# Kernel tuning notes

Hardware: AMD Instinct MI355X
Metric: run time of the kernel (lower is better)

## Reference

```python
import jax, jax.numpy as jnp
import numpy as np

BLOCK_SIZE = 64          # elements per quantization block
SCALER_BLOCK_SIZE = 256  # scalers per double-quantization block
OUT, IN = 11008, 4096
N_BLOCKS = OUT * IN // BLOCK_SIZE          # 704512
N_SCALER_BLOCKS = N_BLOCKS // SCALER_BLOCK_SIZE  # 2752

# QLoRA NF4 (4-bit NormalFloat) codebook
NF4_TABLE = np.array([
    -1.0, -0.6961928009986877, -0.5250730514526367, -0.39491748809814453,
    -0.28444138169288635, -0.18477343022823334, -0.10644006729125977,
    -0.029167551919817924, 0.0, 0.07958029955625534, 0.16093020141124725,
    0.24611230194568634, 0.33791524171829224, 0.44070982933044434,
    0.5626170039176941, 0.7229568362236023], dtype=np.float32)


def setup_inputs() -> dict:
    key = jax.random.key(0)
    k1, k2, k3, k4, k5 = jax.random.split(key, 5)
    x = jax.random.normal(k1, (4, 2048, IN), dtype=jnp.float32)
    # 4-bit codebook indices for each weight element
    qweight = jax.random.randint(k2, (OUT, IN), 0, 16, dtype=jnp.int32)
    # int8-style quantized per-block scalers (positive magnitudes)
    quantized_scalers = jax.random.randint(k3, (N_BLOCKS,), 1, 127, dtype=jnp.int32)
    # per scaler-block quantization factor (strictly positive, away from zero)
    quantization_factor = jax.random.uniform(k4, (N_SCALER_BLOCKS,), dtype=jnp.float32,
                                             minval=0.5, maxval=1.5) * 127.0
    scaler_mean = jax.random.uniform(k5, (1,), dtype=jnp.float32) * 0.01
    return {"x": x, "qweight": qweight, "quantized_scalers": quantized_scalers,
            "quantization_factor": quantization_factor, "scaler_mean": scaler_mean}


def dequantize_nf4(qweight, quantized_scalers, quantization_factor, scaler_mean, dtype):
    table = jnp.asarray(NF4_TABLE, dtype=dtype)
    # double-dequantize the per-block scalers
    scalers = (quantized_scalers.astype(dtype)
               / jnp.repeat(quantization_factor.astype(dtype), SCALER_BLOCK_SIZE)
               + scaler_mean.astype(dtype)[0])                      # [N_BLOCKS]
    # codebook lookup, then per-block scale
    w = table[qweight].reshape(N_BLOCKS, BLOCK_SIZE) * scalers[:, None]
    return w.reshape(OUT, IN)


def reference(x, qweight, quantized_scalers, quantization_factor, scaler_mean):
    # Faithful to LinearNF4.forward: F.linear(x, weight.to(x.dtype))
    w = dequantize_nf4(qweight, quantized_scalers, quantization_factor,
                       scaler_mean, x.dtype)                        # [OUT, IN]
    return jnp.einsum('bsi,oi->bso', x, w)
```

## Files before the change

### kernel.cpp

```cpp
#include <hip/hip_runtime.h>
#include <stdint.h>

#define M_ROWS 8192
#define K_DIM  4096
#define N_DIM  11008
#define KSTEPS (K_DIM / 64)

#define BM 256
#define BN 256
#define MBLKS (M_ROWS / BM)
#define NBLKS (N_DIM / BN)
#define NWG   (MBLKS * NBLKS)

typedef __attribute__((ext_vector_type(4))) float          f32x4;
typedef __attribute__((ext_vector_type(8))) __bf16         bf16x8;
typedef __attribute__((ext_vector_type(4))) int            i32x4;
typedef __attribute__((ext_vector_type(8))) unsigned short u16x8;

__constant__ float NF4_TBL[16] = {
    -1.0f, -0.6961928009986877f, -0.5250730514526367f, -0.39491748809814453f,
    -0.28444138169288635f, -0.18477343022823334f, -0.10644006729125977f,
    -0.029167551919817924f, 0.0f, 0.07958029955625534f, 0.16093020141124725f,
    0.24611230194568634f, 0.33791524171829224f, 0.44070982933044434f,
    0.5626170039176941f, 0.7229568362236023f};

__device__ __forceinline__ unsigned short f2bf(float f) {
  uint32_t u = __float_as_uint(f);
  u += 0x7fffu + ((u >> 16) & 1u);
  return (unsigned short)(u >> 16);
}

__device__ __forceinline__ void gload_lds16(const void* g, const void* l) {
  __builtin_amdgcn_global_load_lds(
      (const __attribute__((address_space(1))) void*)(uintptr_t)g,
      (__attribute__((address_space(3))) void*)(uint32_t)(uintptr_t)l,
      16, 0, 0);
}

__global__ void convert_x_kernel(const float* __restrict__ x,
                                 unsigned short* __restrict__ xb) {
  const long n8 = (long)M_ROWS * K_DIM / 8;
  for (long t = (long)blockIdx.x * blockDim.x + threadIdx.x; t < n8;
       t += (long)gridDim.x * blockDim.x) {
    const float* p = x + t * 8;
    f32x4 v0 = *(const f32x4*)p;
    f32x4 v1 = *(const f32x4*)(p + 4);
    u16x8 o;
    o[0] = f2bf(v0[0]); o[1] = f2bf(v0[1]); o[2] = f2bf(v0[2]); o[3] = f2bf(v0[3]);
    o[4] = f2bf(v1[0]); o[5] = f2bf(v1[1]); o[6] = f2bf(v1[2]); o[7] = f2bf(v1[3]);
    *(u16x8*)(xb + t * 8) = o;
  }
}

__global__ void dequant_w_kernel(const int* __restrict__ qw,
                                 const int* __restrict__ qs,
                                 const float* __restrict__ qf,
                                 const float* __restrict__ mean,
                                 unsigned short* __restrict__ wb) {
  __shared__ float tbl[16];
  if (threadIdx.x < 16) tbl[threadIdx.x] = NF4_TBL[threadIdx.x];
  __syncthreads();
  const float mu = mean[0];
  const long n8 = (long)N_DIM * K_DIM / 8;
  for (long t = (long)blockIdx.x * blockDim.x + threadIdx.x; t < n8;
       t += (long)gridDim.x * blockDim.x) {
    long f = t * 8;
    int  g = (int)(f >> 6);
    float s = (float)qs[g] / qf[g >> 8] + mu;
    i32x4 q0 = *(const i32x4*)(qw + f);
    i32x4 q1 = *(const i32x4*)(qw + f + 4);
    u16x8 o;
    o[0] = f2bf(tbl[q0[0]] * s); o[1] = f2bf(tbl[q0[1]] * s);
    o[2] = f2bf(tbl[q0[2]] * s); o[3] = f2bf(tbl[q0[3]] * s);
    o[4] = f2bf(tbl[q1[0]] * s); o[5] = f2bf(tbl[q1[1]] * s);
    o[6] = f2bf(tbl[q1[2]] * s); o[7] = f2bf(tbl[q1[3]] * s);
    *(u16x8*)(wb + f) = o;
  }
}

#define STG(GP, LB)                                                              \
  gload_lds16((GP) + (long)srow * K_DIM + scol, &LDSbuf[(LB) + wid * 1024]);     \
  gload_lds16((GP) + (long)(64 + srow) * K_DIM + scol,                           \
              &LDSbuf[(LB) + 8192 + wid * 1024]);

#define SB __builtin_amdgcn_sched_barrier(0)

#define RD_A2(DST, MB, SA)                                                        \
  DST[0][0] = *(const bf16x8*)&LDSbuf[(SA) + aoff + (MB) * 2048 + kswz0];         \
  DST[0][1] = *(const bf16x8*)&LDSbuf[(SA) + aoff + (MB) * 2048 + kswz1];         \
  DST[1][0] = *(const bf16x8*)&LDSbuf[(SA) + aoff + ((MB) + 1) * 2048 + kswz0];   \
  DST[1][1] = *(const bf16x8*)&LDSbuf[(SA) + aoff + ((MB) + 1) * 2048 + kswz1];

#define RD_B2(NB, CB)                                                             \
  bq[NB][0]     = *(const bf16x8*)&LDSbuf[(CB) + boff + (NB) * 2048 + kswz0];     \
  bq[NB][1]     = *(const bf16x8*)&LDSbuf[(CB) + boff + (NB) * 2048 + kswz1];     \
  bq[NB + 1][0] = *(const bf16x8*)&LDSbuf[(CB) + boff + ((NB) + 1) * 2048 + kswz0];\
  bq[NB + 1][1] = *(const bf16x8*)&LDSbuf[(CB) + boff + ((NB) + 1) * 2048 + kswz1];

#define MFP(MI, AF, AI, NI)                                                       \
  acc[MI][NI] = __builtin_amdgcn_mfma_f32_16x16x32_bf16(AF[AI][0], bq[NI][0], acc[MI][NI], 0, 0, 0); \
  acc[MI][NI] = __builtin_amdgcn_mfma_f32_16x16x32_bf16(AF[AI][1], bq[NI][1], acc[MI][NI], 0, 0, 0);

#define TILE_BODY(BASE)                                                           \
    RD_A2(af_a, ((BASE) + 0) & 7, sAr);                                           \
    RD_B2(0, cB);                                                                 \
    SB;                                                                           \
    RD_B2(2, cB);                                                                 \
    STG(wb + n0g * K_DIM + kB, nB);                                               \
    __builtin_amdgcn_s_setprio(1);                                                \
    MFP(((BASE) + 0) & 7, af_a, 0, 0) MFP(((BASE) + 1) & 7, af_a, 1, 0)           \
    MFP(((BASE) + 0) & 7, af_a, 0, 1) MFP(((BASE) + 1) & 7, af_a, 1, 1)           \
    __builtin_amdgcn_s_setprio(0);                                                \
    SB;                                                                           \
    RD_A2(af_b, ((BASE) + 2) & 7, sAr);                                           \
    STG(wb + (n0g + 128) * K_DIM + kB, nB + 16384);                               \
    __builtin_amdgcn_s_setprio(1);                                                \
    MFP(((BASE) + 0) & 7, af_a, 0, 2) MFP(((BASE) + 1) & 7, af_a, 1, 2)           \
    MFP(((BASE) + 0) & 7, af_a, 0, 3) MFP(((BASE) + 1) & 7, af_a, 1, 3)           \
    __builtin_amdgcn_s_setprio(0);                                                \
    SB;                                                                           \
    STG(xb + m0g * K_DIM + kA, sAs);                                              \
    __builtin_amdgcn_s_setprio(1);                                                \
    MFP(((BASE) + 2) & 7, af_b, 0, 2) MFP(((BASE) + 3) & 7, af_b, 1, 2)           \
    MFP(((BASE) + 2) & 7, af_b, 0, 3) MFP(((BASE) + 3) & 7, af_b, 1, 3)           \
    __builtin_amdgcn_s_setprio(0);                                                \
    SB;                                                                           \
    RD_A2(af_a, ((BASE) + 4) & 7, sAr);                                           \
    STG(xb + (m0g + 128) * K_DIM + kA, sAs + 16384);                              \
    __builtin_amdgcn_s_setprio(1);                                                \
    MFP(((BASE) + 2) & 7, af_b, 0, 0) MFP(((BASE) + 3) & 7, af_b, 1, 0)           \
    MFP(((BASE) + 2) & 7, af_b, 0, 1) MFP(((BASE) + 3) & 7, af_b, 1, 1)           \
    __builtin_amdgcn_s_setprio(0);                                                \
    SB;                                                                           \
    __builtin_amdgcn_s_setprio(1);                                                \
    MFP(((BASE) + 4) & 7, af_a, 0, 0) MFP(((BASE) + 5) & 7, af_a, 1, 0)           \
    MFP(((BASE) + 4) & 7, af_a, 0, 1) MFP(((BASE) + 5) & 7, af_a, 1, 1)           \
    __builtin_amdgcn_s_setprio(0);                                                \
    SB;                                                                           \
    RD_A2(af_b, ((BASE) + 6) & 7, sAr);                                           \
    __builtin_amdgcn_s_setprio(1);                                                \
    MFP(((BASE) + 4) & 7, af_a, 0, 2) MFP(((BASE) + 5) & 7, af_a, 1, 2)           \
    MFP(((BASE) + 4) & 7, af_a, 0, 3) MFP(((BASE) + 5) & 7, af_a, 1, 3)           \
    __builtin_amdgcn_s_setprio(0);                                                \
    SB;                                                                           \
    __builtin_amdgcn_s_setprio(1);                                                \
    MFP(((BASE) + 6) & 7, af_b, 0, 2) MFP(((BASE) + 7) & 7, af_b, 1, 2)           \
    MFP(((BASE) + 6) & 7, af_b, 0, 3) MFP(((BASE) + 7) & 7, af_b, 1, 3)           \
    __builtin_amdgcn_s_setprio(0);                                                \
    SB;                                                                           \
    __builtin_amdgcn_s_setprio(1);                                                \
    MFP(((BASE) + 6) & 7, af_b, 0, 0) MFP(((BASE) + 7) & 7, af_b, 1, 0)           \
    MFP(((BASE) + 6) & 7, af_b, 0, 1) MFP(((BASE) + 7) & 7, af_b, 1, 1)           \
    __builtin_amdgcn_s_setprio(0);

#define TILE_SETUP                                                                \
    const int cur = t & 1;                                                        \
    const int cB = 98304 + cur * 32768;                                           \
    const int nB = 98304 + (cur ^ 1) * 32768;                                     \
    const long kB = (long)((t + 1 < KSTEPS ? t + 1 : KSTEPS - 1) * 64);           \
    const long kA = (long)((t + 2 < KSTEPS ? t + 2 : KSTEPS - 1) * 64);

#define TILE_BOUND                                                                \
    asm volatile("s_waitcnt vmcnt(4)");                                           \
    __builtin_amdgcn_sched_barrier(0);                                            \
    __builtin_amdgcn_s_barrier();                                                 \
    __builtin_amdgcn_sched_barrier(0);                                            \
    int tmp = sAr; sAr = sAn; sAn = sAs; sAs = tmp;

__global__ __launch_bounds__(512, 2) void gemm_pipe(
    const unsigned short* __restrict__ xb, const unsigned short* __restrict__ wb,
    float* __restrict__ C) {
  __align__(16) __shared__ unsigned char LDSbuf[163840];

  const int tid = threadIdx.x;
  const int wid = tid >> 6, lane = tid & 63;
  const int wr = wid >> 2, wc = wid & 3;
  const int r16 = lane & 15, hi = lane >> 4;

  const int p = ((int)blockIdx.x & 7) * (NWG / 8) + ((int)blockIdx.x >> 3);
  int mb, nb;
  if (p < 1280) {
    const int nbg = p >> 7;
    const int rem = p & 127;
    const int mbg = rem >> 5;
    const int s   = rem & 31;
    mb = mbg * 8 + (s & 7);
    nb = nbg * 4 + (s >> 3);
  } else {
    const int q   = p - 1280;
    const int mbg = q / 24;
    const int s   = q % 24;
    mb = mbg * 8 + (s & 7);
    nb = 40 + (s >> 3);
  }
  const long m0g = (long)mb * BM, n0g = (long)nb * BN;

  const int srow = wid * 8 + (lane >> 3);
  const int scol = ((lane & 7) ^ (lane >> 3)) * 8;

  const int aoff = (wr * 128 + r16) * 128;
  const int boff = (wc * 64 + r16) * 128;
  const int kswz0 = ((hi ^ (r16 & 7)) << 4);
  const int kswz1 = kswz0 ^ 64;

  STG(xb + m0g * K_DIM,              0);
  STG(xb + (m0g + 128) * K_DIM,      16384);
  STG(wb + n0g * K_DIM,              98304);
  STG(wb + (n0g + 128) * K_DIM,      98304 + 16384);
  STG(xb + m0g * K_DIM + 64,         32768);
  STG(xb + (m0g + 128) * K_DIM + 64, 32768 + 16384);
  asm volatile("s_waitcnt vmcnt(4)");
  __builtin_amdgcn_sched_barrier(0);
  __builtin_amdgcn_s_barrier();

  bf16x8 af_a[2][2], af_b[2][2], bq[4][2];
  f32x4 acc[8][4] = {};

  int sAr = 0, sAn = 32768, sAs = 65536;

  if ((wid & 1) == 0) {
    for (int t = 0; t < KSTEPS; ++t) {
      TILE_SETUP
      TILE_BODY(0)
      TILE_BOUND
    }
  } else {
    for (int t = 0; t < KSTEPS; ++t) {
      TILE_SETUP
      TILE_BODY(4)
      TILE_BOUND
    }
  }

  const long crow = m0g + wr * 128 + hi * 4;
  const long ccol = n0g + wc * 64 + r16;
#pragma unroll
  for (int m = 0; m < 8; ++m)
#pragma unroll
    for (int n = 0; n < 4; ++n)
#pragma unroll
      for (int r = 0; r < 4; ++r)
        __builtin_nontemporal_store(
            acc[m][n][r], &C[(crow + m * 16 + r) * N_DIM + ccol + n * 16]);
}

__global__ __launch_bounds__(256) void gemm_fallback(
    const float* __restrict__ Xf, const int* __restrict__ qw,
    const int* __restrict__ qs, const float* __restrict__ qf,
    const float* __restrict__ meanp, float* __restrict__ C) {
  __shared__ unsigned short As[128 * 64];
  __shared__ unsigned short Bs[128 * 64];
  __shared__ float tbl[16];
  const int tid = threadIdx.x;
  if (tid < 16) tbl[tid] = NF4_TBL[tid];
  const float mu = meanp[0];
  const int nwg = (M_ROWS / 128) * (N_DIM / 128);
  const int wg = ((int)blockIdx.x & 7) * (nwg / 8) + ((int)blockIdx.x >> 3);
  const int mbf = wg % (M_ROWS / 128), nbf = wg / (M_ROWS / 128);
  const int m0 = mbf * 128, n0 = nbf * 128;
  const int wid = tid >> 6, lane = tid & 63;
  const int wrf = wid >> 1, wcc = wid & 1;
  const int r16 = lane & 15, hi = lane >> 4;
  f32x4 acc[4][4] = {};
  for (int t = 0; t < KSTEPS; ++t) {
    const int k0 = t * 64;
    __syncthreads();
#pragma unroll
    for (int i = 0; i < 4; ++i) {
      int gi = i * 256 + tid;
      int row = gi >> 3, kq = (gi & 7) * 8;
      const float* px = Xf + (long)(m0 + row) * K_DIM + k0 + kq;
      f32x4 v0 = *(const f32x4*)px;
      f32x4 v1 = *(const f32x4*)(px + 4);
      u16x8 o;
      o[0] = f2bf(v0[0]); o[1] = f2bf(v0[1]); o[2] = f2bf(v0[2]); o[3] = f2bf(v0[3]);
      o[4] = f2bf(v1[0]); o[5] = f2bf(v1[1]); o[6] = f2bf(v1[2]); o[7] = f2bf(v1[3]);
      *(u16x8*)&As[row * 64 + kq] = o;
    }
#pragma unroll
    for (int i = 0; i < 4; ++i) {
      int gi = i * 256 + tid;
      int row = gi >> 3, kq = (gi & 7) * 8;
      const int* pq = qw + (long)(n0 + row) * K_DIM + k0 + kq;
      i32x4 q0 = *(const i32x4*)pq;
      i32x4 q1 = *(const i32x4*)(pq + 4);
      int g = (n0 + row) * (K_DIM / 64) + t;
      float s = (float)qs[g] / qf[g >> 8] + mu;
      u16x8 o;
      o[0] = f2bf(tbl[q0[0]] * s); o[1] = f2bf(tbl[q0[1]] * s);
      o[2] = f2bf(tbl[q0[2]] * s); o[3] = f2bf(tbl[q0[3]] * s);
      o[4] = f2bf(tbl[q1[0]] * s); o[5] = f2bf(tbl[q1[1]] * s);
      o[6] = f2bf(tbl[q1[2]] * s); o[7] = f2bf(tbl[q1[3]] * s);
      *(u16x8*)&Bs[row * 64 + kq] = o;
    }
    __syncthreads();
    bf16x8 afr[4][2], bfr[4][2];
#pragma unroll
    for (int i = 0; i < 4; ++i)
#pragma unroll
      for (int h = 0; h < 2; ++h) {
        afr[i][h] = *(const bf16x8*)&As[(wrf * 64 + i * 16 + r16) * 64 + h * 32 + hi * 8];
        bfr[i][h] = *(const bf16x8*)&Bs[(wcc * 64 + i * 16 + r16) * 64 + h * 32 + hi * 8];
      }
#pragma unroll
    for (int i = 0; i < 4; ++i)
#pragma unroll
      for (int j = 0; j < 4; ++j) {
        acc[i][j] = __builtin_amdgcn_mfma_f32_16x16x32_bf16(afr[i][0], bfr[j][0], acc[i][j], 0, 0, 0);
        acc[i][j] = __builtin_amdgcn_mfma_f32_16x16x32_bf16(afr[i][1], bfr[j][1], acc[i][j], 0, 0, 0);
      }
  }
  const int crow = m0 + wrf * 64 + hi * 4;
  const int ccol = n0 + wcc * 64 + r16;
#pragma unroll
  for (int i = 0; i < 4; ++i)
#pragma unroll
    for (int j = 0; j < 4; ++j)
#pragma unroll
      for (int r = 0; r < 4; ++r)
        C[(long)(crow + i * 16 + r) * N_DIM + (ccol + j * 16)] = acc[i][j][r];
}

extern "C" void kernel_launch(void* const* d_in, const int* in_sizes, int n_in,
                              void* d_out, int out_size, void* d_ws, size_t ws_size,
                              hipStream_t stream) {
  const float* x    = (const float*)d_in[0];
  const int*   qw   = (const int*)d_in[1];
  const int*   qs   = (const int*)d_in[2];
  const float* qf   = (const float*)d_in[3];
  const float* mean = (const float*)d_in[4];
  float* out = (float*)d_out;

  const size_t xb_bytes = (size_t)M_ROWS * K_DIM * 2;
  const size_t wb_bytes = (size_t)N_DIM * K_DIM * 2;

  if (ws_size >= xb_bytes + wb_bytes) {
    unsigned short* xb = (unsigned short*)d_ws;
    unsigned short* wb = (unsigned short*)((char*)d_ws + xb_bytes);
    convert_x_kernel<<<4096, 256, 0, stream>>>(x, xb);
    dequant_w_kernel<<<4096, 256, 0, stream>>>(qw, qs, qf, mean, wb);
    gemm_pipe<<<NWG, 512, 0, stream>>>(xb, wb, out);
  } else {
    gemm_fallback<<<(M_ROWS / 128) * (N_DIM / 128), 256, 0, stream>>>(
        x, qw, qs, qf, mean, out);
  }
}
```

Before: 689.2 us.

## Switch main GEMM loop from 16x16x32 to 32x32x16 bf16 MFMA tiles

Replaces the 16x16x32 MFMA instructions in the pipelined GEMM with 32x32x16 MFMA, restructuring the LDS fragment reads, swizzle indexing, accumulator layout (4x2 f32x16) and output store mapping to match. The larger MFMA shape needs fewer LDS fragment reads per FLOP and fewer instructions issued. The risks are higher register pressure from the 16-wide accumulators, possible LDS bank conflicts under the new swizzle, and correctness of the new row/column mapping.

Result: slower. 758.8 us (+10.1%).

```diff
diff --git a/kernel.cpp b/kernel.cpp
--- a/kernel.cpp
+++ b/kernel.cpp
@@ -12,10 +12,11 @@
 #define NBLKS (N_DIM / BN)
 #define NWG   (MBLKS * NBLKS)
 
-typedef __attribute__((ext_vector_type(4))) float          f32x4;
-typedef __attribute__((ext_vector_type(8))) __bf16         bf16x8;
-typedef __attribute__((ext_vector_type(4))) int            i32x4;
-typedef __attribute__((ext_vector_type(8))) unsigned short u16x8;
+typedef __attribute__((ext_vector_type(4)))  float          f32x4;
+typedef __attribute__((ext_vector_type(16))) float          f32x16;
+typedef __attribute__((ext_vector_type(8)))  __bf16         bf16x8;
+typedef __attribute__((ext_vector_type(4)))  int            i32x4;
+typedef __attribute__((ext_vector_type(8)))  unsigned short u16x8;
 
 __constant__ float NF4_TBL[16] = {
     -1.0f, -0.6961928009986877f, -0.5250730514526367f, -0.39491748809814453f,
@@ -85,72 +86,70 @@
 
 #define SB __builtin_amdgcn_sched_barrier(0)
 
-#define RD_A2(DST, MB, SA)                                                        \
-  DST[0][0] = *(const bf16x8*)&LDSbuf[(SA) + aoff + (MB) * 2048 + kswz0];         \
-  DST[0][1] = *(const bf16x8*)&LDSbuf[(SA) + aoff + (MB) * 2048 + kswz1];         \
-  DST[1][0] = *(const bf16x8*)&LDSbuf[(SA) + aoff + ((MB) + 1) * 2048 + kswz0];   \
-  DST[1][1] = *(const bf16x8*)&LDSbuf[(SA) + aoff + ((MB) + 1) * 2048 + kswz1];
-
-#define RD_B2(NB, CB)                                                             \
-  bq[NB][0]     = *(const bf16x8*)&LDSbuf[(CB) + boff + (NB) * 2048 + kswz0];     \
-  bq[NB][1]     = *(const bf16x8*)&LDSbuf[(CB) + boff + (NB) * 2048 + kswz1];     \
-  bq[NB + 1][0] = *(const bf16x8*)&LDSbuf[(CB) + boff + ((NB) + 1) * 2048 + kswz0];\
-  bq[NB + 1][1] = *(const bf16x8*)&LDSbuf[(CB) + boff + ((NB) + 1) * 2048 + kswz1];
-
-#define MFP(MI, AF, AI, NI)                                                       \
-  acc[MI][NI] = __builtin_amdgcn_mfma_f32_16x16x32_bf16(AF[AI][0], bq[NI][0], acc[MI][NI], 0, 0, 0); \
-  acc[MI][NI] = __builtin_amdgcn_mfma_f32_16x16x32_bf16(AF[AI][1], bq[NI][1], acc[MI][NI], 0, 0, 0);
+#define KB(KS) (((((KS) * 2 + lid5) ^ l7) << 4))
+
+#define RD_A32(DST, MH, KS, SA)                                                   \
+  DST[0] = *(const bf16x8*)&LDSbuf[(SA) + aoffB + ((MH) * 2 + 0) * 4096 + KB(KS)];\
+  DST[1] = *(const bf16x8*)&LDSbuf[(SA) + aoffB + ((MH) * 2 + 1) * 4096 + KB(KS)];
+
+#define RD_B32(DST, KS, CB)                                                       \
+  DST[0] = *(const bf16x8*)&LDSbuf[(CB) + boffB + 0 * 4096 + KB(KS)];             \
+  DST[1] = *(const bf16x8*)&LDSbuf[(CB) + boffB + 1 * 4096 + KB(KS)];
+
+#define CL32(MH, AF, BQ)                                                          \
+  acc[(MH) * 2 + 0][0] = __builtin_amdgcn_mfma_f32_32x32x16_bf16(AF[0], BQ[0], acc[(MH) * 2 + 0][0], 0, 0, 0); \
+  acc[(MH) * 2 + 1][0] = __builtin_amdgcn_mfma_f32_32x32x16_bf16(AF[1], BQ[0], acc[(MH) * 2 + 1][0], 0, 0, 0); \
+  acc[(MH) * 2 + 0][1] = __builtin_amdgcn_mfma_f32_32x32x16_bf16(AF[0], BQ[1], acc[(MH) * 2 + 0][1], 0, 0, 0); \
+  acc[(MH) * 2 + 1][1] = __builtin_amdgcn_mfma_f32_32x32x16_bf16(AF[1], BQ[1], acc[(MH) * 2 + 1][1], 0, 0, 0);
 
 #define TILE_BODY(BASE)                                                           \
-    RD_A2(af_a, ((BASE) + 0) & 7, sAr);                                           \
-    RD_B2(0, cB);                                                                 \
-    SB;                                                                           \
-    RD_B2(2, cB);                                                                 \
+    RD_A32(af_a, 0, (((BASE) >> 1) + 0) & 3, sAr);                                \
+    RD_B32(bq_c, (((BASE) >> 1) + 0) & 3, cB);                                    \
+    SB;                                                                           \
+    RD_A32(af_b, 1, (((BASE) >> 1) + 0) & 3, sAr);                                \
     STG(wb + n0g * K_DIM + kB, nB);                                               \
     __builtin_amdgcn_s_setprio(1);                                                \
-    MFP(((BASE) + 0) & 7, af_a, 0, 0) MFP(((BASE) + 1) & 7, af_a, 1, 0)           \
-    MFP(((BASE) + 0) & 7, af_a, 0, 1) MFP(((BASE) + 1) & 7, af_a, 1, 1)           \
-    __builtin_amdgcn_s_setprio(0);                                                \
-    SB;                                                                           \
-    RD_A2(af_b, ((BASE) + 2) & 7, sAr);                                           \
+    CL32(0, af_a, bq_c)                                                           \
+    __builtin_amdgcn_s_setprio(0);                                                \
+    SB;                                                                           \
+    RD_A32(af_a, 0, (((BASE) >> 1) + 1) & 3, sAr);                                \
+    RD_B32(bq_n, (((BASE) >> 1) + 1) & 3, cB);                                    \
     STG(wb + (n0g + 128) * K_DIM + kB, nB + 16384);                               \
     __builtin_amdgcn_s_setprio(1);                                                \
-    MFP(((BASE) + 0) & 7, af_a, 0, 2) MFP(((BASE) + 1) & 7, af_a, 1, 2)           \
-    MFP(((BASE) + 0) & 7, af_a, 0, 3) MFP(((BASE) + 1) & 7, af_a, 1, 3)           \
-    __builtin_amdgcn_s_setprio(0);                                                \
-    SB;                                                                           \
+    CL32(1, af_b, bq_c)                                                           \
+    __builtin_amdgcn_s_setprio(0);                                                \
+    SB;                                                                           \
+    RD_A32(af_b, 1, (((BASE) >> 1) + 1) & 3, sAr);                                \
     STG(xb + m0g * K_DIM + kA, sAs);                                              \
     __builtin_amdgcn_s_setprio(1);                                                \
-    MFP(((BASE) + 2) & 7, af_b, 0, 2) MFP(((BASE) + 3) & 7, af_b, 1, 2)           \
-    MFP(((BASE) + 2) & 7, af_b, 0, 3) MFP(((BASE) + 3) & 7, af_b, 1, 3)           \
-    __builtin_amdgcn_s_setprio(0);                                                \
-    SB;                                                                           \
-    RD_A2(af_a, ((BASE) + 4) & 7, sAr);                                           \
+    CL32(0, af_a, bq_n)                                                           \
+    __builtin_amdgcn_s_setprio(0);                                                \
+    SB;                                                                           \
+    RD_A32(af_a, 0, (((BASE) >> 1) + 2) & 3, sAr);                                \
+    RD_B32(bq_c, (((BASE) >> 1) + 2) & 3, cB);                                    \
     STG(xb + (m0g + 128) * K_DIM + kA, sAs + 16384);                              \
     __builtin_amdgcn_s_setprio(1);                                                \
-    MFP(((BASE) + 2) & 7, af_b, 0, 0) MFP(((BASE) + 3) & 7, af_b, 1, 0)           \
-    MFP(((BASE) + 2) & 7, af_b, 0, 1) MFP(((BASE) + 3) & 7, af_b, 1, 1)           \
-    __builtin_amdgcn_s_setprio(0);                                                \
-    SB;                                                                           \
-    __builtin_amdgcn_s_setprio(1);                                                \
-    MFP(((BASE) + 4) & 7, af_a, 0, 0) MFP(((BASE) + 5) & 7, af_a, 1, 0)           \
-    MFP(((BASE) + 4) & 7, af_a, 0, 1) MFP(((BASE) + 5) & 7, af_a, 1, 1)           \
-    __builtin_amdgcn_s_setprio(0);                                                \
-    SB;                                                                           \
-    RD_A2(af_b, ((BASE) + 6) & 7, sAr);                                           \
-    __builtin_amdgcn_s_setprio(1);                                                \
-    MFP(((BASE) + 4) & 7, af_a, 0, 2) MFP(((BASE) + 5) & 7, af_a, 1, 2)           \
-    MFP(((BASE) + 4) & 7, af_a, 0, 3) MFP(((BASE) + 5) & 7, af_a, 1, 3)           \
-    __builtin_amdgcn_s_setprio(0);                                                \
-    SB;                                                                           \
-    __builtin_amdgcn_s_setprio(1);                                                \
-    MFP(((BASE) + 6) & 7, af_b, 0, 2) MFP(((BASE) + 7) & 7, af_b, 1, 2)           \
-    MFP(((BASE) + 6) & 7, af_b, 0, 3) MFP(((BASE) + 7) & 7, af_b, 1, 3)           \
-    __builtin_amdgcn_s_setprio(0);                                                \
-    SB;                                                                           \
-    __builtin_amdgcn_s_setprio(1);                                                \
-    MFP(((BASE) + 6) & 7, af_b, 0, 0) MFP(((BASE) + 7) & 7, af_b, 1, 0)           \
-    MFP(((BASE) + 6) & 7, af_b, 0, 1) MFP(((BASE) + 7) & 7, af_b, 1, 1)           \
+    CL32(1, af_b, bq_n)                                                           \
+    __builtin_amdgcn_s_setprio(0);                                                \
+    SB;                                                                           \
+    RD_A32(af_b, 1, (((BASE) >> 1) + 2) & 3, sAr);                                \
+    __builtin_amdgcn_s_setprio(1);                                                \
+    CL32(0, af_a, bq_c)                                                           \
+    __builtin_amdgcn_s_setprio(0);                                                \
+    SB;                                                                           \
+    RD_A32(af_a, 0, (((BASE) >> 1) + 3) & 3, sAr);                                \
+    RD_B32(bq_n, (((BASE) >> 1) + 3) & 3, cB);                                    \
+    __builtin_amdgcn_s_setprio(1);                                                \
+    CL32(1, af_b, bq_c)                                                           \
+    __builtin_amdgcn_s_setprio(0);                                                \
+    SB;                                                                           \
+    RD_A32(af_b, 1, (((BASE) >> 1) + 3) & 3, sAr);                                \
+    __builtin_amdgcn_s_setprio(1);                                                \
+    CL32(0, af_a, bq_n)                                                           \
+    __builtin_amdgcn_s_setprio(0);                                                \
+    SB;                                                                           \
+    __builtin_amdgcn_s_setprio(1);                                                \
+    CL32(1, af_b, bq_n)                                                           \
     __builtin_amdgcn_s_setprio(0);
 
 #define TILE_SETUP                                                                \
@@ -175,7 +174,7 @@
   const int tid = threadIdx.x;
   const int wid = tid >> 6, lane = tid & 63;
   const int wr = wid >> 2, wc = wid & 3;
-  const int r16 = lane & 15, hi = lane >> 4;
+  const int l31 = lane & 31, lid5 = lane >> 5, l7 = lane & 7;
 
   const int p = ((int)blockIdx.x & 7) * (NWG / 8) + ((int)blockIdx.x >> 3);
   int mb, nb;
@@ -198,10 +197,8 @@
   const int srow = wid * 8 + (lane >> 3);
   const int scol = ((lane & 7) ^ (lane >> 3)) * 8;
 
-  const int aoff = (wr * 128 + r16) * 128;
-  const int boff = (wc * 64 + r16) * 128;
-  const int kswz0 = ((hi ^ (r16 & 7)) << 4);
-  const int kswz1 = kswz0 ^ 64;
+  const int aoffB = (wr * 128 + l31) * 128;
+  const int boffB = (wc * 64 + l31) * 128;
 
   STG(xb + m0g * K_DIM,              0);
   STG(xb + (m0g + 128) * K_DIM,      16384);
@@ -213,8 +210,8 @@
   __builtin_amdgcn_sched_barrier(0);
   __builtin_amdgcn_s_barrier();
 
-  bf16x8 af_a[2][2], af_b[2][2], bq[4][2];
-  f32x4 acc[8][4] = {};
+  bf16x8 af_a[2], af_b[2], bq_c[2], bq_n[2];
+  f32x16 acc[4][2] = {};
 
   int sAr = 0, sAn = 32768, sAs = 65536;
 
@@ -232,16 +229,19 @@
     }
   }
 
-  const long crow = m0g + wr * 128 + hi * 4;
-  const long ccol = n0g + wc * 64 + r16;
-#pragma unroll
-  for (int m = 0; m < 8; ++m)
-#pragma unroll
-    for (int n = 0; n < 4; ++n)
-#pragma unroll
-      for (int r = 0; r < 4; ++r)
+  const long crow = m0g + wr * 128;
+  const long ccol = n0g + wc * 64 + l31;
+#pragma unroll
+  for (int mi = 0; mi < 4; ++mi)
+#pragma unroll
+    for (int ni = 0; ni < 2; ++ni)
+#pragma unroll
+      for (int reg = 0; reg < 16; ++reg) {
+        const int row = (reg & 3) + 8 * (reg >> 2) + 4 * lid5;
         __builtin_nontemporal_store(
-            acc[m][n][r], &C[(crow + m * 16 + r) * N_DIM + ccol + n * 16]);
+            acc[mi][ni][reg],
+            &C[(crow + mi * 32 + row) * N_DIM + ccol + ni * 32]);
+      }
 }
 
 __global__ __launch_bounds__(256) void gemm_fallback(
```
